# Optimization experiments

Hardware: AMD Instinct MI355X
Metric: run time of the kernel (lower is better)

The kernel has to match this reference:

```python
import jax, jax.numpy as jnp
import numpy as np

NEG = -1e9  # matches torch masked_fill value -1000000000.0


def setup_inputs() -> dict:
    key = jax.random.key(0)
    ks = jax.random.split(key, 8)
    B, n, m, d = 16, 1024, 128, 768
    C = jax.random.normal(ks[0], (B, n, d), jnp.float32)
    Q = jax.random.normal(ks[1], (B, m, d), jnp.float32)
    c_mask = jax.random.randint(ks[2], (B, 1, n), 0, 2).astype(bool)
    q_mask = jax.random.randint(ks[3], (B, 1, m), 0, 2).astype(bool)
    w1 = jax.random.normal(ks[4], (d,), jnp.float32)
    w2 = jax.random.normal(ks[5], (d,), jnp.float32)
    w3 = jax.random.normal(ks[6], (1, 1, d), jnp.float32)
    bias = jax.random.normal(ks[7], (1, 1), jnp.float32)
    return {"C": C, "Q": Q, "c_mask": c_mask, "q_mask": q_mask,
            "w1": w1, "w2": w2, "w3": w3, "bias": bias}


def reference(C, Q, c_mask, q_mask, w1, w2, w3, bias):
    # trilinear score S[b,i,j] = w1.C_i + w2.Q_j + (C_i * w3) . Q_j
    c_logit = jnp.einsum('bnd,d->bn', C, w1)[:, :, None]      # [B,n,1]
    q_logit = jnp.einsum('bmd,d->bm', Q, w2)[:, None, :]      # [B,1,m]
    dot_logit = jnp.einsum('bnd,bmd->bnm', C * w3, Q)         # [B,n,m]
    S = c_logit + q_logit + dot_logit                          # [B,n,m]

    # C2Q: mask padded query cols and padded context rows, softmax over query dim
    Sm = jnp.where(q_mask, NEG, S)                             # q_mask [B,1,m]
    Sm = jnp.where(jnp.swapaxes(c_mask, 1, 2), NEG, Sm)        # c_mask^T [B,n,1]
    C2Q = jax.nn.softmax(Sm, axis=-1)                          # [B,n,m]

    # Q2C: mask context cols of S^T, max over query dim, softmax over context dim
    St = jnp.where(c_mask, NEG, jnp.swapaxes(S, 1, 2))         # [B,m,n]
    q2c_logits = jnp.max(St, axis=1, keepdims=True)            # [B,1,n]
    Q2C = jax.nn.softmax(q2c_logits, axis=-1)                  # [B,1,n]

    A = jnp.einsum('bnm,bmd->bnd', C2Q, Q)                     # [B,n,d]
    # torch expands Q2C to [B,n,n] then bmm's with C; every row is identical,
    # so compute once and broadcast: [B,1,n] @ [B,n,d] -> [B,1,d]
    Bctx = jnp.einsum('bon,bnd->bod', Q2C, C)                  # [B,1,d]
    Bfull = jnp.broadcast_to(Bctx, C.shape)
    out = jnp.concatenate([C, A, C * A, C * Bfull], axis=-1)   # [B,n,4d]
    return out
```

## Files before the change

kernel.cpp:

```cpp
#include <hip/hip_runtime.h>
#include <math.h>
#include <stdint.h>

#define NEGV -1e9f
typedef float f32x4 __attribute__((ext_vector_type(4)));
typedef short bf16x8 __attribute__((ext_vector_type(8)));
typedef unsigned int u32x4 __attribute__((ext_vector_type(4)));

constexpr int B_ = 16, N_ = 1024, M_ = 128, D_ = 768;
constexpr int NCH = 12;

constexpr size_t OFF_QLOGP = 0;
constexpr size_t OFF_ROWMAX = 98304;
constexpr size_t OFF_BCTX   = 163840;
constexpr size_t OFF_WQ2C   = 212992;
constexpr size_t OFF_QIMG   = 278528;
constexpr size_t SZ_QIMG    = 3145728;
constexpr size_t WS_NEED    = OFF_QIMG + 4 * SZ_QIMG;

__device__ __forceinline__ unsigned short bf_rne(float x) {
    unsigned u = __float_as_uint(x);
    return (unsigned short)((u + 0x7fffu + ((u >> 16) & 1u)) >> 16);
}
__device__ __forceinline__ void splitf(float x, unsigned short& h, unsigned short& l) {
    unsigned short hb = bf_rne(x);
    float hf = __uint_as_float((unsigned)hb << 16);
    h = hb;
    l = bf_rne(x - hf);
}
__device__ __forceinline__ void gl_lds16(const void* g, void* l) {
    __builtin_amdgcn_global_load_lds(
        (const __attribute__((address_space(1))) void*)g,
        (__attribute__((address_space(3))) void*)l, 16, 0, 0);
}

__global__ __launch_bounds__(256) void k_prep(const float* __restrict__ Q,
                                              const float* __restrict__ w2,
                                              const float* __restrict__ w3,
                                              char* __restrict__ qwh, char* __restrict__ qwl,
                                              char* __restrict__ qth, char* __restrict__ qtl,
                                              float* __restrict__ qlogp) {
    int b = blockIdx.x / NCH, c = blockIdx.x % NCH;
    int t = threadIdx.x;
    __shared__ unsigned sT[128][66];
    __shared__ float sW2[64], sW3c[64];
    if (t < 64) sW2[t] = w2[c * 64 + t];
    else if (t < 128) sW3c[t - 64] = w3[c * 64 + (t - 64)];
    __syncthreads();
    int j = t >> 1, half = t & 1;
    const float* src = Q + ((size_t)(b * M_ + j)) * D_ + c * 64 + half * 32;
    unsigned short hs[32], ls[32];
    float qsum = 0.f;
#pragma unroll
    for (int u = 0; u < 8; ++u) {
        float4 v = *(const float4*)(src + u * 4);
        float f[4] = {v.x, v.y, v.z, v.w};
#pragma unroll
        for (int e = 0; e < 4; ++e) {
            int idx = u * 4 + e, d = half * 32 + idx;
            qsum += f[e] * sW2[d];
            unsigned short rh, rl; splitf(f[e], rh, rl);
            sT[j][d] = ((unsigned)rh << 16) | (unsigned)rl;
            unsigned short h, l; splitf(f[e] * sW3c[d], h, l);
            hs[idx] = h; ls[idx] = l;
        }
    }
    qsum += __shfl_xor(qsum, 1);
    if (half == 0) qlogp[(size_t)(b * M_ + j) * NCH + c] = qsum;
    size_t cb = ((size_t)(b * NCH + c)) * 16384;
    {
        int jh = j >> 6, jt = (j >> 4) & 3, c15j = j & 15;
#pragma unroll
        for (int u2 = 0; u2 < 4; ++u2) {
            int g = half * 4 + u2, ks = g >> 2, q4g = g & 3;
            int lane = q4g * 16 + c15j;
            bf16x8 hv, lv;
#pragma unroll
            for (int e = 0; e < 8; ++e) { hv[e] = (short)hs[u2 * 8 + e]; lv[e] = (short)ls[u2 * 8 + e]; }
            size_t off = cb + (size_t)((((jh * 2 + ks) * 4 + jt) * 64 + lane) * 16);
            *(bf16x8*)(qwh + off) = hv;
            *(bf16x8*)(qwl + off) = lv;
        }
    }
    __syncthreads();
#pragma unroll
    for (int u = 0; u < 4; ++u) {
        int id = t * 4 + u;
        int dd = id >> 4, gj = id & 15;
        int jh3 = dd >> 5, dt = (dd >> 4) & 1, c15q = dd & 15;
        int ks2 = gj >> 2, q4g = gj & 3;
        int lane = q4g * 16 + c15q;
        bf16x8 hv, lv;
#pragma unroll
        for (int e = 0; e < 8; ++e) {
            unsigned p = sT[gj * 8 + e][dd];
            hv[e] = (short)(p >> 16); lv[e] = (short)(p & 0xffffu);
        }
        size_t off = cb + (size_t)((((jh3 * 4 + ks2) * 2 + dt) * 64 + lane) * 16);
        *(bf16x8*)(qth + off) = hv;
        *(bf16x8*)(qtl + off) = lv;
    }
}

__global__ __launch_bounds__(256, 3) void k_main_v8(const float* __restrict__ C,
                                                    const int* __restrict__ c_mask,
                                                    const int* __restrict__ q_mask,
                                                    const float* __restrict__ w1,
                                                    const float* __restrict__ qlogp,
                                                    const char* __restrict__ qwh,
                                                    const char* __restrict__ qwl,
                                                    const char* __restrict__ qth,
                                                    const char* __restrict__ qtl,
                                                    float* __restrict__ rowmax,
                                                    float* __restrict__ out) {
    const int bid = (blockIdx.x & 7) * 64 + (blockIdx.x >> 3);
    const int b  = bid >> 5;
    const int r0 = (bid & 31) * 32;
    const int t  = threadIdx.x;
    const int wv = t >> 6, lane = t & 63;
    const int rg = wv >> 1, jh = wv & 1;
    const int q4 = lane >> 4, c15 = t & 15;

    const float* Cb = C + ((size_t)(b * N_ + r0)) * D_;

    __shared__ __align__(16) char uni[49152];
    __shared__ float sW1[D_];
    __shared__ float sQlog[M_];
    __shared__ int   sQmask[M_];
    __shared__ float sClog[32];
    __shared__ float sRedR[64], sRedM[64], sRedS[64];

    char* sQH  = uni;
    char* sQL  = uni + 16384;
    char* sQtH = uni;
    char* sQtL = uni + 16384;
    char* sPH  = uni + 32768;
    char* sPL  = uni + 40960;

    for (int k = t; k < D_; k += 256) sW1[k] = w1[k];
    if (t < M_) {
        const float* qp = qlogp + (size_t)(b * M_ + t) * NCH;
        float4 x = *(const float4*)qp, y = *(const float4*)(qp + 4), z = *(const float4*)(qp + 8);
        sQlog[t] = ((x.x + x.y) + (x.z + x.w)) + ((y.x + y.y) + (y.z + y.w)) +
                   ((z.x + z.y) + (z.z + z.w));
        sQmask[t] = q_mask[b * M_ + t];
    }
    __syncthreads();

    f32x4 acc[4] = {};
    float clogp = 0.f;
    const int arow = rg * 16 + c15;
    const float* CbA = Cb + (size_t)arow * D_;
    const size_t qcb = (size_t)(b * NCH) * 16384;

    for (int kidx = 0; kidx < NCH; ++kidx) {
        __syncthreads();
        {
            size_t gb = qcb + (size_t)kidx * 16384;
#pragma unroll
            for (int it = 0; it < 4; ++it) {
                int qo = it * 4096 + wv * 1024;
                gl_lds16(qwh + gb + qo + lane * 16, sQH + qo);
                gl_lds16(qwl + gb + qo + lane * 16, sQL + qo);
            }
        }
        bf16x8 ah[2], al[2];
        const int kb = kidx * 64;
#pragma unroll
        for (int ks = 0; ks < 2; ++ks) {
            const int k0 = kb + (ks * 4 + q4) * 8;
            float4 ca  = *(const float4*)(CbA + k0);
            float4 cb2 = *(const float4*)(CbA + k0 + 4);
            float cc[8] = {ca.x, ca.y, ca.z, ca.w, cb2.x, cb2.y, cb2.z, cb2.w};
#pragma unroll
            for (int e = 0; e < 8; ++e) {
                clogp += cc[e] * sW1[k0 + e];
                unsigned short h, l; splitf(cc[e], h, l);
                ah[ks][e] = (short)h; al[ks][e] = (short)l;
            }
        }
        __syncthreads();
#pragma unroll
        for (int ks = 0; ks < 2; ++ks) {
#pragma unroll
            for (int jt = 0; jt < 4; ++jt) {
                int fo = (((jh * 2 + ks) * 4 + jt) * 64 + lane) * 16;
                bf16x8 bh = *(const bf16x8*)(sQH + fo);
                bf16x8 bl = *(const bf16x8*)(sQL + fo);
                acc[jt] = __builtin_amdgcn_mfma_f32_16x16x32_bf16(ah[ks], bh, acc[jt], 0, 0, 0);
                acc[jt] = __builtin_amdgcn_mfma_f32_16x16x32_bf16(ah[ks], bl, acc[jt], 0, 0, 0);
                acc[jt] = __builtin_amdgcn_mfma_f32_16x16x32_bf16(al[ks], bh, acc[jt], 0, 0, 0);
            }
        }
    }
    clogp += __shfl_xor(clogp, 16);
    clogp += __shfl_xor(clogp, 32);
    if (jh == 0 && q4 == 0) sClog[arow] = clogp;
    __syncthreads();

    float qlg[4]; int qmv[4];
#pragma unroll
    for (int jt = 0; jt < 4; ++jt) {
        int j = jh * 64 + jt * 16 + c15;
        qlg[jt] = sQlog[j]; qmv[jt] = sQmask[j];
    }
    int cmv[4]; float clgr[4];
#pragma unroll
    for (int rr = 0; rr < 4; ++rr) {
        int row = rg * 16 + q4 * 4 + rr;
        cmv[rr]  = c_mask[b * N_ + r0 + row];
        clgr[rr] = sClog[row];
    }
    float mv[4][4], rmx[4], mmx[4];
#pragma unroll
    for (int rr = 0; rr < 4; ++rr) { rmx[rr] = -INFINITY; mmx[rr] = -INFINITY; }
#pragma unroll
    for (int jt = 0; jt < 4; ++jt)
#pragma unroll
        for (int rr = 0; rr < 4; ++rr) {
            float val = acc[jt][rr] + clgr[rr] + qlg[jt];
            float m   = (cmv[rr] | qmv[jt]) ? NEGV : val;
            mv[jt][rr] = m;
            rmx[rr] = fmaxf(rmx[rr], val);
            mmx[rr] = fmaxf(mmx[rr], m);
        }
#pragma unroll
    for (int rr = 0; rr < 4; ++rr)
#pragma unroll
        for (int off = 8; off; off >>= 1) {
            rmx[rr] = fmaxf(rmx[rr], __shfl_xor(rmx[rr], off));
            mmx[rr] = fmaxf(mmx[rr], __shfl_xor(mmx[rr], off));
        }
    if (c15 == 0) {
#pragma unroll
        for (int rr = 0; rr < 4; ++rr) {
            int row = rg * 16 + q4 * 4 + rr;
            sRedR[row * 2 + jh] = rmx[rr];
            sRedM[row * 2 + jh] = mmx[rr];
        }
    }
    __syncthreads();
    float Mm[4], sum[4];
#pragma unroll
    for (int rr = 0; rr < 4; ++rr) {
        int row = rg * 16 + q4 * 4 + rr;
        float Mraw = fmaxf(sRedR[row * 2], sRedR[row * 2 + 1]);
        Mm[rr] = fmaxf(sRedM[row * 2], sRedM[row * 2 + 1]);
        if (jh == 0 && c15 == 0) rowmax[b * N_ + r0 + row] = Mraw;
        sum[rr] = 0.f;
    }
    float p[4][4];
#pragma unroll
    for (int jt = 0; jt < 4; ++jt)
#pragma unroll
        for (int rr = 0; rr < 4; ++rr) {
            float e = __expf(mv[jt][rr] - Mm[rr]);
            p[jt][rr] = e; sum[rr] += e;
        }
#pragma unroll
    for (int rr = 0; rr < 4; ++rr) {
#pragma unroll
        for (int off = 8; off; off >>= 1) sum[rr] += __shfl_xor(sum[rr], off);
        if (c15 == 0) sRedS[(rg * 16 + q4 * 4 + rr) * 2 + jh] = sum[rr];
    }
    __syncthreads();
#pragma unroll
    for (int rr = 0; rr < 4; ++rr) {
        int row = rg * 16 + q4 * 4 + rr;
        float inv = 1.f / (sRedS[row * 2] + sRedS[row * 2 + 1]);
#pragma unroll
        for (int jt = 0; jt < 4; ++jt) {
            float P = p[jt][rr] * inv;
            unsigned short h, l; splitf(P, h, l);
            int j = jh * 64 + jt * 16 + c15;
            int addr = row * 256 + (((j >> 3) ^ (row & 7)) * 16) + (j & 7) * 2;
            *(short*)(sPH + addr) = (short)h;
            *(short*)(sPL + addr) = (short)l;
        }
    }
    __syncthreads();

    bf16x8 pah[4], pal[4];
    const int prow = rg * 16 + c15;
#pragma unroll
    for (int ks2 = 0; ks2 < 4; ++ks2) {
        int gja = ks2 * 4 + q4;
        int pgp = (gja ^ (prow & 7)) * 16;
        pah[ks2] = *(const bf16x8*)(sPH + prow * 256 + pgp);
        pal[ks2] = *(const bf16x8*)(sPL + prow * 256 + pgp);
    }
    for (int dc = 0; dc < NCH; ++dc) {
        __syncthreads();
        {
            size_t gb = qcb + (size_t)dc * 16384;
#pragma unroll
            for (int it = 0; it < 4; ++it) {
                int qo = it * 4096 + wv * 1024;
                gl_lds16(qth + gb + qo + lane * 16, sQtH + qo);
                gl_lds16(qtl + gb + qo + lane * 16, sQtL + qo);
            }
        }
        __syncthreads();
        f32x4 acc2[2] = {};
#pragma unroll
        for (int ks2 = 0; ks2 < 4; ++ks2) {
#pragma unroll
            for (int dt = 0; dt < 2; ++dt) {
                int fo = (((jh * 4 + ks2) * 2 + dt) * 64 + lane) * 16;
                bf16x8 bh = *(const bf16x8*)(sQtH + fo);
                bf16x8 bl = *(const bf16x8*)(sQtL + fo);
                acc2[dt] = __builtin_amdgcn_mfma_f32_16x16x32_bf16(pah[ks2], bh, acc2[dt], 0, 0, 0);
                acc2[dt] = __builtin_amdgcn_mfma_f32_16x16x32_bf16(pah[ks2], bl, acc2[dt], 0, 0, 0);
                acc2[dt] = __builtin_amdgcn_mfma_f32_16x16x32_bf16(pal[ks2], bh, acc2[dt], 0, 0, 0);
            }
        }
#pragma unroll
        for (int dt = 0; dt < 2; ++dt) {
            int dcol = dc * 64 + jh * 32 + dt * 16 + c15;
#pragma unroll
            for (int rr = 0; rr < 4; ++rr) {
                int row = rg * 16 + q4 * 4 + rr;
                float a = acc2[dt][rr];
                float c = Cb[(size_t)row * D_ + dcol];
                size_t ob = (size_t)(b * N_ + r0 + row) * 3072;
                out[ob + dcol] = c;
                out[ob + 768 + dcol] = a;
                out[ob + 1536 + dcol] = c * a;
            }
        }
    }
}

__global__ __launch_bounds__(256) void k_q2c(const float* __restrict__ rowmax,
                                             const int* __restrict__ c_mask,
                                             float* __restrict__ wq2c) {
    int b = blockIdx.x, t = threadIdx.x;
    __shared__ float red[8];
    float l[4];
#pragma unroll
    for (int u = 0; u < 4; ++u) {
        int i = t + u * 256;
        l[u] = (c_mask[b * N_ + i] != 0) ? NEGV : rowmax[b * N_ + i];
    }
    float mx = fmaxf(fmaxf(l[0], l[1]), fmaxf(l[2], l[3]));
#pragma unroll
    for (int off = 32; off; off >>= 1) mx = fmaxf(mx, __shfl_xor(mx, off));
    if ((t & 63) == 0) red[t >> 6] = mx;
    __syncthreads();
    mx = fmaxf(fmaxf(red[0], red[1]), fmaxf(red[2], red[3]));
    float e[4], s = 0.f;
#pragma unroll
    for (int u = 0; u < 4; ++u) { e[u] = __expf(l[u] - mx); s += e[u]; }
#pragma unroll
    for (int off = 32; off; off >>= 1) s += __shfl_xor(s, off);
    if ((t & 63) == 0) red[4 + (t >> 6)] = s;
    __syncthreads();
    s = red[4] + red[5] + red[6] + red[7];
    float inv = 1.f / s;
#pragma unroll
    for (int u = 0; u < 4; ++u) wq2c[b * N_ + t + u * 256] = e[u] * inv;
}

__global__ __launch_bounds__(256) void k_bctx(const float* __restrict__ C,
                                              const float* __restrict__ wq2c,
                                              float* __restrict__ Bctx) {
    int b  = blockIdx.x / 12;
    int c0 = (blockIdx.x % 12) * 64;
    int t  = threadIdx.x;
    int col = t & 63, ig = t >> 6;
    __shared__ float part[4][64];
    const float* wb = wq2c + b * N_;
    const float* Cb = C + (size_t)b * N_ * D_;
    float s = 0.f;
    for (int i = ig * 256; i < ig * 256 + 256; ++i)
        s += wb[i] * Cb[(size_t)i * D_ + c0 + col];
    part[ig][col] = s;
    __syncthreads();
    if (t < 64) Bctx[b * D_ + c0 + t] = part[0][t] + part[1][t] + part[2][t] + part[3][t];
}

__global__ __launch_bounds__(192) void k_final(const float* __restrict__ C,
                                               const float* __restrict__ Bctx,
                                               float* __restrict__ out) {
    int row = blockIdx.x;
    int b = row >> 10;
    int t = threadIdx.x;
    float4 c = *(const float4*)(C + (size_t)row * D_ + t * 4);
    float4 g = *(const float4*)(Bctx + (size_t)b * D_ + t * 4);
    *(float4*)(out + (size_t)row * 3072 + 2304 + t * 4) =
        make_float4(c.x * g.x, c.y * g.y, c.z * g.z, c.w * g.w);
}

__global__ __launch_bounds__(256) void k_qlogit(const float* __restrict__ Q,
                                                const float* __restrict__ w2,
                                                float* __restrict__ qlog) {
    int idx  = blockIdx.x * 4 + (threadIdx.x >> 6);
    int lane = threadIdx.x & 63;
    const float* q = Q + (size_t)idx * D_;
    float s = 0.f;
    for (int k = lane; k < D_; k += 64) s += q[k] * w2[k];
#pragma unroll
    for (int off = 32; off; off >>= 1) s += __shfl_xor(s, off);
    if (lane == 0) qlog[idx] = s;
}

__global__ __launch_bounds__(256, 2) void k_main_fb(const float* __restrict__ C,
                                                    const float* __restrict__ Q,
                                                    const int* __restrict__ c_mask,
                                                    const int* __restrict__ q_mask,
                                                    const float* __restrict__ w1,
                                                    const float* __restrict__ w3,
                                                    const float* __restrict__ qlog,
                                                    float* __restrict__ rowmax,
                                                    float* __restrict__ out) {
    const int bid = (blockIdx.x & 7) * 64 + (blockIdx.x >> 3);
    const int b  = bid >> 5;
    const int r0 = (bid & 31) * 32;
    const int t  = threadIdx.x;
    const int wv = t >> 6;
    const int rg = wv >> 1, jh = wv & 1;
    const int q4 = (t & 63) >> 4, c15 = t & 15;

    const float* Cb = C + ((size_t)(b * N_ + r0)) * D_;
    const float* Qb = Q + (size_t)b * M_ * D_;

    __shared__ __align__(16) char uni[49152];
    __shared__ float sW1[D_], sW3[D_];
    __shared__ float sQlog[M_];
    __shared__ int   sQmask[M_];
    __shared__ float sClog[32];
    __shared__ float sRedR[64], sRedM[64], sRedS[64];

    char* sCwH = uni;
    char* sCwL = uni + 4096;
    char* sQH  = uni + 8192;
    char* sQL  = uni + 24576;
    char* sPt  = uni;
    char* sQtP = uni + 16384;

    for (int k = t; k < D_; k += 256) { sW1[k] = w1[k]; sW3[k] = w3[k]; }
    if (t < M_) { sQlog[t] = qlog[b * M_ + t]; sQmask[t] = q_mask[b * M_ + t]; }

    f32x4 acc[4] = {};
    float clog = 0.f;
    const int cr = t >> 3, ckq = t & 7;
    const int qj = t >> 1, qk0 = (t & 1) * 32;

    for (int kb = 0; kb < D_; kb += 64) {
        __syncthreads();
        {
            const float* p = Cb + (size_t)cr * D_ + kb + ckq * 8;
            float4 a  = *(const float4*)p;
            float4 bb = *(const float4*)(p + 4);
            float cc[8] = {a.x, a.y, a.z, a.w, bb.x, bb.y, bb.z, bb.w};
            bf16x8 hv, lv;
            int kk = kb + ckq * 8;
#pragma unroll
            for (int e = 0; e < 8; ++e) {
                clog += cc[e] * sW1[kk + e];
                unsigned short h, l;
                splitf(cc[e] * sW3[kk + e], h, l);
                hv[e] = (short)h; lv[e] = (short)l;
            }
            int pg = (ckq ^ (cr & 7)) * 16;
            *(bf16x8*)(sCwH + cr * 128 + pg) = hv;
            *(bf16x8*)(sCwL + cr * 128 + pg) = lv;
        }
        {
            const float* p = Qb + (size_t)qj * D_ + kb + qk0;
#pragma unroll
            for (int u = 0; u < 4; ++u) {
                float4 a  = *(const float4*)(p + u * 8);
                float4 bb = *(const float4*)(p + u * 8 + 4);
                float qq[8] = {a.x, a.y, a.z, a.w, bb.x, bb.y, bb.z, bb.w};
                bf16x8 hv, lv;
#pragma unroll
                for (int e = 0; e < 8; ++e) {
                    unsigned short h, l;
                    splitf(qq[e], h, l);
                    hv[e] = (short)h; lv[e] = (short)l;
                }
                int g  = (t & 1) * 4 + u;
                int pg = (g ^ (qj & 7)) * 16;
                *(bf16x8*)(sQH + qj * 128 + pg) = hv;
                *(bf16x8*)(sQL + qj * 128 + pg) = lv;
            }
        }
        __syncthreads();
        const int arow = rg * 16 + c15;
#pragma unroll
        for (int ks = 0; ks < 2; ++ks) {
            int g  = ks * 4 + q4;
            int pg = (g ^ (c15 & 7)) * 16;
            bf16x8 ah = *(const bf16x8*)(sCwH + arow * 128 + pg);
            bf16x8 al = *(const bf16x8*)(sCwL + arow * 128 + pg);
#pragma unroll
            for (int jt = 0; jt < 4; ++jt) {
                int jr = jh * 64 + jt * 16 + c15;
                bf16x8 bh = *(const bf16x8*)(sQH + jr * 128 + pg);
                bf16x8 bl = *(const bf16x8*)(sQL + jr * 128 + pg);
                acc[jt] = __builtin_amdgcn_mfma_f32_16x16x32_bf16(ah, bh, acc[jt], 0, 0, 0);
                acc[jt] = __builtin_amdgcn_mfma_f32_16x16x32_bf16(ah, bl, acc[jt], 0, 0, 0);
                acc[jt] = __builtin_amdgcn_mfma_f32_16x16x32_bf16(al, bh, acc[jt], 0, 0, 0);
            }
        }
    }

    clog += __shfl_xor(clog, 1); clog += __shfl_xor(clog, 2); clog += __shfl_xor(clog, 4);
    if ((t & 7) == 0) sClog[cr] = clog;
    __syncthreads();

    float qlg[4]; int qmv[4];
#pragma unroll
    for (int jt = 0; jt < 4; ++jt) {
        int j = jh * 64 + jt * 16 + c15;
        qlg[jt] = sQlog[j]; qmv[jt] = sQmask[j];
    }
    int cmv[4]; float clgr[4];
#pragma unroll
    for (int rr = 0; rr < 4; ++rr) {
        int row = rg * 16 + q4 * 4 + rr;
        cmv[rr]  = c_mask[b * N_ + r0 + row];
        clgr[rr] = sClog[row];
    }
    float mv[4][4], rmx[4], mmx[4];
#pragma unroll
    for (int rr = 0; rr < 4; ++rr) { rmx[rr] = -INFINITY; mmx[rr] = -INFINITY; }
#pragma unroll
    for (int jt = 0; jt < 4; ++jt)
#pragma unroll
        for (int rr = 0; rr < 4; ++rr) {
            float val = acc[jt][rr] + clgr[rr] + qlg[jt];
            float m   = (cmv[rr] | qmv[jt]) ? NEGV : val;
            mv[jt][rr] = m;
            rmx[rr] = fmaxf(rmx[rr], val);
            mmx[rr] = fmaxf(mmx[rr], m);
        }
#pragma unroll
    for (int rr = 0; rr < 4; ++rr)
#pragma unroll
        for (int off = 8; off; off >>= 1) {
            rmx[rr] = fmaxf(rmx[rr], __shfl_xor(rmx[rr], off));
            mmx[rr] = fmaxf(mmx[rr], __shfl_xor(mmx[rr], off));
        }
    if (c15 == 0) {
#pragma unroll
        for (int rr = 0; rr < 4; ++rr) {
            int row = rg * 16 + q4 * 4 + rr;
            sRedR[row * 2 + jh] = rmx[rr];
            sRedM[row * 2 + jh] = mmx[rr];
        }
    }
    __syncthreads();
    float Mm[4], sum[4];
#pragma unroll
    for (int rr = 0; rr < 4; ++rr) {
        int row = rg * 16 + q4 * 4 + rr;
        float Mraw = fmaxf(sRedR[row * 2], sRedR[row * 2 + 1]);
        Mm[rr] = fmaxf(sRedM[row * 2], sRedM[row * 2 + 1]);
        if (jh == 0 && c15 == 0) rowmax[b * N_ + r0 + row] = Mraw;
        sum[rr] = 0.f;
    }
    float p[4][4];
#pragma unroll
    for (int jt = 0; jt < 4; ++jt)
#pragma unroll
        for (int rr = 0; rr < 4; ++rr) {
            float e = __expf(mv[jt][rr] - Mm[rr]);
            p[jt][rr] = e; sum[rr] += e;
        }
#pragma unroll
    for (int rr = 0; rr < 4; ++rr) {
#pragma unroll
        for (int off = 8; off; off >>= 1) sum[rr] += __shfl_xor(sum[rr], off);
        if (c15 == 0) sRedS[(rg * 16 + q4 * 4 + rr) * 2 + jh] = sum[rr];
    }
    __syncthreads();
#pragma unroll
    for (int rr = 0; rr < 4; ++rr) {
        int row = rg * 16 + q4 * 4 + rr;
        float inv = 1.f / (sRedS[row * 2] + sRedS[row * 2 + 1]);
#pragma unroll
        for (int jt = 0; jt < 4; ++jt) {
            float P = p[jt][rr] * inv;
            unsigned short h, l; splitf(P, h, l);
            unsigned pk = ((unsigned)h << 16) | (unsigned)l;
            int j  = jh * 64 + jt * 16 + c15;
            int gu = j >> 2;
            *(unsigned*)(sPt + row * 512 + ((gu ^ (row & 7)) * 16) + (j & 3) * 4) = pk;
        }
    }

    const int pj = t >> 1, pdh = (t & 1) * 32;
    for (int d0 = 0; d0 < D_; d0 += 64) {
        __syncthreads();
        {
            const float* p = Qb + (size_t)pj * D_ + d0 + pdh;
            int gu = pj >> 2, joff = (pj & 3) * 4;
#pragma unroll
            for (int u = 0; u < 8; ++u) {
                float4 a = *(const float4*)(p + u * 4);
                float qq[4] = {a.x, a.y, a.z, a.w};
#pragma unroll
                for (int e = 0; e < 4; ++e) {
                    unsigned short h, l; splitf(qq[e], h, l);
                    int d = pdh + u * 4 + e;
                    *(unsigned*)(sQtP + d * 512 + ((gu ^ (d & 7)) * 16) + joff) =
                        ((unsigned)h << 16) | (unsigned)l;
                }
            }
        }
        __syncthreads();
        f32x4 acc2[2] = {};
        const int prow = rg * 16 + c15;
#pragma unroll
        for (int ks2 = 0; ks2 < 4; ++ks2) {
            int gu0 = ks2 * 8 + q4 * 2;
            u32x4 pa = *(const u32x4*)(sPt + prow * 512 + ((gu0 ^ (c15 & 7)) * 16));
            u32x4 pb = *(const u32x4*)(sPt + prow * 512 + (((gu0 + 1) ^ (c15 & 7)) * 16));
            bf16x8 phi, plo;
#pragma unroll
            for (int e = 0; e < 4; ++e) {
                phi[e]     = (short)(pa[e] >> 16); plo[e]     = (short)(pa[e] & 0xffffu);
                phi[e + 4] = (short)(pb[e] >> 16); plo[e + 4] = (short)(pb[e] & 0xffffu);
            }
#pragma unroll
            for (int dt = 0; dt < 2; ++dt) {
                int dr = jh * 32 + dt * 16 + c15;
                u32x4 qa = *(const u32x4*)(sQtP + dr * 512 + ((gu0 ^ (dr & 7)) * 16));
                u32x4 qb = *(const u32x4*)(sQtP + dr * 512 + (((gu0 + 1) ^ (dr & 7)) * 16));
                bf16x8 bh, bl;
#pragma unroll
                for (int e = 0; e < 4; ++e) {
                    bh[e]     = (short)(qa[e] >> 16); bl[e]     = (short)(qa[e] & 0xffffu);
                    bh[e + 4] = (short)(qb[e] >> 16); bl[e + 4] = (short)(qb[e] & 0xffffu);
                }
                acc2[dt] = __builtin_amdgcn_mfma_f32_16x16x32_bf16(phi, bh, acc2[dt], 0, 0, 0);
                acc2[dt] = __builtin_amdgcn_mfma_f32_16x16x32_bf16(phi, bl, acc2[dt], 0, 0, 0);
                acc2[dt] = __builtin_amdgcn_mfma_f32_16x16x32_bf16(plo, bh, acc2[dt], 0, 0, 0);
            }
        }
#pragma unroll
        for (int dt = 0; dt < 2; ++dt)
#pragma unroll
            for (int rr = 0; rr < 4; ++rr) {
                int row  = rg * 16 + q4 * 4 + rr;
                int dcol = d0 + jh * 32 + dt * 16 + c15;
                float a = acc2[dt][rr];
                float c = Cb[(size_t)row * D_ + dcol];
                size_t ob = (size_t)(b * N_ + r0 + row) * 3072;
                out[ob + dcol] = c;
                out[ob + 768 + dcol] = a;
                out[ob + 1536 + dcol] = c * a;
            }
    }
}

extern "C" void kernel_launch(void* const* d_in, const int* in_sizes, int n_in,
                              void* d_out, int out_size, void* d_ws, size_t ws_size,
                              hipStream_t stream) {
    const float* C      = (const float*)d_in[0];
    const float* Q      = (const float*)d_in[1];
    const int*   c_mask = (const int*)d_in[2];
    const int*   q_mask = (const int*)d_in[3];
    const float* w1     = (const float*)d_in[4];
    const float* w2     = (const float*)d_in[5];
    const float* w3     = (const float*)d_in[6];
    float* out = (float*)d_out;
    char*  wsb = (char*)d_ws;

    float* qlogp  = (float*)(wsb + OFF_QLOGP);
    float* rowmax = (float*)(wsb + OFF_ROWMAX);
    float* bctx   = (float*)(wsb + OFF_BCTX);
    float* wq2c   = (float*)(wsb + OFF_WQ2C);

    if (ws_size >= WS_NEED) {
        char* qwh = wsb + OFF_QIMG;
        char* qwl = qwh + SZ_QIMG;
        char* qth = qwl + SZ_QIMG;
        char* qtl = qth + SZ_QIMG;
        k_prep<<<B_ * NCH, 256, 0, stream>>>(Q, w2, w3, qwh, qwl, qth, qtl, qlogp);
        k_main_v8<<<512, 256, 0, stream>>>(C, c_mask, q_mask, w1, qlogp,
                                           qwh, qwl, qth, qtl, rowmax, out);
    } else {
        float* qlog = (float*)(wsb + OFF_QLOGP);
        k_qlogit<<<512, 256, 0, stream>>>(Q, w2, qlog);
        k_main_fb<<<512, 256, 0, stream>>>(C, Q, c_mask, q_mask, w1, w3, qlog, rowmax, out);
    }
    k_q2c<<<16, 256, 0, stream>>>(rowmax, c_mask, wq2c);
    k_bctx<<<192, 256, 0, stream>>>(C, wq2c, bctx);
    k_final<<<16384, 192, 0, stream>>>(C, bctx, out);
}
```

Measured before the change: 112.5 us.

## Split main kernel and fuse Q2C softmax and C*Bctx output into pipeline

The main kernel is split in two. The first half computes scores and the C2Q probabilities, then writes the probability tile to workspace along with per-tile partial Q2C softmax sums (local max, denominator, weighted C rows). A small combine kernel merges the 32 partials per batch into Bctx with an online-softmax rescale. The second half reloads the probabilities, computes A, and writes all four output slices, including C*Bctx. This removes the separate k_q2c, k_bctx and k_final passes, which re-read C and rewrote a quarter of the output, at the cost of an extra kernel boundary and a round trip of the probability tile through global memory.

```diff
diff --git a/kernel.cpp b/kernel.cpp
--- a/kernel.cpp
+++ b/kernel.cpp
@@ -10,11 +10,13 @@
 constexpr int B_ = 16, N_ = 1024, M_ = 128, D_ = 768;
 constexpr int NCH = 12;
 
-constexpr size_t OFF_QLOGP = 0;
-constexpr size_t OFF_ROWMAX = 98304;
-constexpr size_t OFF_BCTX   = 163840;
+constexpr size_t OFF_QLOGP  = 0;
+constexpr size_t OFF_BCTX   = 98304;
+constexpr size_t OFF_PART   = 147456;
+constexpr size_t OFF_ROWMAX = 147456;
 constexpr size_t OFF_WQ2C   = 212992;
-constexpr size_t OFF_QIMG   = 278528;
+constexpr size_t OFF_PIMG   = 2244608;
+constexpr size_t OFF_QIMG   = 10633216;
 constexpr size_t SZ_QIMG    = 3145728;
 constexpr size_t WS_NEED    = OFF_QIMG + 4 * SZ_QIMG;
 
@@ -102,17 +104,15 @@
     }
 }
 
-__global__ __launch_bounds__(256, 3) void k_main_v8(const float* __restrict__ C,
-                                                    const int* __restrict__ c_mask,
-                                                    const int* __restrict__ q_mask,
-                                                    const float* __restrict__ w1,
-                                                    const float* __restrict__ qlogp,
-                                                    const char* __restrict__ qwh,
-                                                    const char* __restrict__ qwl,
-                                                    const char* __restrict__ qth,
-                                                    const char* __restrict__ qtl,
-                                                    float* __restrict__ rowmax,
-                                                    float* __restrict__ out) {
+__global__ __launch_bounds__(256, 3) void k_main1(const float* __restrict__ C,
+                                                  const int* __restrict__ c_mask,
+                                                  const int* __restrict__ q_mask,
+                                                  const float* __restrict__ w1,
+                                                  const float* __restrict__ qlogp,
+                                                  const char* __restrict__ qwh,
+                                                  const char* __restrict__ qwl,
+                                                  float* __restrict__ part,
+                                                  char* __restrict__ pimg) {
     const int bid = (blockIdx.x & 7) * 64 + (blockIdx.x >> 3);
     const int b  = bid >> 5;
     const int r0 = (bid & 31) * 32;
@@ -124,18 +124,16 @@
     const float* Cb = C + ((size_t)(b * N_ + r0)) * D_;
 
     __shared__ __align__(16) char uni[49152];
-    __shared__ float sW1[D_];
     __shared__ float sQlog[M_];
     __shared__ int   sQmask[M_];
-    __shared__ float sClog[32];
+    __shared__ float sClog[32], sMraw[32], sMl[32], sWr[32];
     __shared__ float sRedR[64], sRedM[64], sRedS[64];
 
-    char* sQH  = uni;
-    char* sQL  = uni + 16384;
-    char* sQtH = uni;
-    char* sQtL = uni + 16384;
-    char* sPH  = uni + 32768;
-    char* sPL  = uni + 40960;
+    char* sQH = uni;
+    char* sQL = uni + 16384;
+    char* sPH = uni + 32768;
+    char* sPL = uni + 40960;
+    float* sW1 = (float*)(uni + 32768);
 
     for (int k = t; k < D_; k += 256) sW1[k] = w1[k];
     if (t < M_) {
@@ -246,7 +244,7 @@
         int row = rg * 16 + q4 * 4 + rr;
         float Mraw = fmaxf(sRedR[row * 2], sRedR[row * 2 + 1]);
         Mm[rr] = fmaxf(sRedM[row * 2], sRedM[row * 2 + 1]);
-        if (jh == 0 && c15 == 0) rowmax[b * N_ + r0 + row] = Mraw;
+        if (jh == 0 && c15 == 0) sMraw[row] = Mraw;
         sum[rr] = 0.f;
     }
     float p[4][4];
@@ -280,6 +278,97 @@
     }
     __syncthreads();
 
+    if (t < 32) sMl[t] = (c_mask[b * N_ + r0 + t] != 0) ? NEGV : sMraw[t];
+    __syncthreads();
+    float lm = -INFINITY;
+#pragma unroll
+    for (int r = 0; r < 32; ++r) lm = fmaxf(lm, sMl[r]);
+    if (t < 32) sWr[t] = __expf(sMl[t] - lm);
+    __syncthreads();
+    float den = 0.f;
+#pragma unroll
+    for (int r = 0; r < 32; ++r) den += sWr[r];
+    {
+        float a0 = 0.f, a1 = 0.f, a2 = 0.f;
+        for (int r = 0; r < 32; ++r) {
+            float w = sWr[r];
+            const float* cr = Cb + (size_t)r * D_;
+            a0 += w * cr[t]; a1 += w * cr[t + 256]; a2 += w * cr[t + 512];
+        }
+        float* slot = part + (size_t)bid * 1024;
+        slot[2 + t] = a0; slot[2 + t + 256] = a1; slot[2 + t + 512] = a2;
+        if (t == 0) { slot[0] = lm; slot[1] = den; }
+    }
+#pragma unroll
+    for (int i = 0; i < 2; ++i) {
+        *(u32x4*)(pimg + (size_t)bid * 16384 + t * 32 + i * 16) =
+            *(const u32x4*)(sPH + t * 32 + i * 16);
+        *(u32x4*)(pimg + (size_t)bid * 16384 + 8192 + t * 32 + i * 16) =
+            *(const u32x4*)(sPL + t * 32 + i * 16);
+    }
+}
+
+__global__ __launch_bounds__(256) void k_combine(const float* __restrict__ part,
+                                                 float* __restrict__ bctx) {
+    int b = blockIdx.x, t = threadIdx.x;
+    __shared__ float sLm[32], sDen[32], sSc[32];
+    if (t < 32) {
+        const float* s = part + (size_t)(b * 32 + t) * 1024;
+        sLm[t] = s[0]; sDen[t] = s[1];
+    }
+    __syncthreads();
+    float gm = -INFINITY;
+#pragma unroll
+    for (int r = 0; r < 32; ++r) gm = fmaxf(gm, sLm[r]);
+    if (t < 32) sSc[t] = __expf(sLm[t] - gm);
+    __syncthreads();
+    float Ds = 0.f;
+#pragma unroll
+    for (int r = 0; r < 32; ++r) Ds += sDen[r] * sSc[r];
+    float inv = 1.f / Ds;
+#pragma unroll
+    for (int u = 0; u < 3; ++u) {
+        int col = t + u * 256;
+        float a = 0.f;
+        for (int rt = 0; rt < 32; ++rt)
+            a += sSc[rt] * part[(size_t)(b * 32 + rt) * 1024 + 2 + col];
+        bctx[b * D_ + col] = a * inv;
+    }
+}
+
+__global__ __launch_bounds__(256, 3) void k_main2(const float* __restrict__ C,
+                                                  const float* __restrict__ bctx,
+                                                  const char* __restrict__ qth,
+                                                  const char* __restrict__ qtl,
+                                                  const char* __restrict__ pimg,
+                                                  float* __restrict__ out) {
+    const int bid = (blockIdx.x & 7) * 64 + (blockIdx.x >> 3);
+    const int b  = bid >> 5;
+    const int r0 = (bid & 31) * 32;
+    const int t  = threadIdx.x;
+    const int wv = t >> 6, lane = t & 63;
+    const int rg = wv >> 1, jh = wv & 1;
+    const int q4 = lane >> 4, c15 = t & 15;
+
+    const float* Cb = C + ((size_t)(b * N_ + r0)) * D_;
+
+    __shared__ __align__(16) char uni[49152];
+    char* sQtH = uni;
+    char* sQtL = uni + 16384;
+    char* sPH  = uni + 32768;
+    char* sPL  = uni + 40960;
+
+    {
+        const char* ps = pimg + (size_t)bid * 16384;
+#pragma unroll
+        for (int it = 0; it < 2; ++it) {
+            int off = it * 4096 + wv * 1024;
+            gl_lds16(ps + off + lane * 16, sPH + off);
+            gl_lds16(ps + 8192 + off + lane * 16, sPL + off);
+        }
+    }
+    __syncthreads();
+
     bf16x8 pah[4], pal[4];
     const int prow = rg * 16 + c15;
 #pragma unroll
@@ -289,6 +378,8 @@
         pah[ks2] = *(const bf16x8*)(sPH + prow * 256 + pgp);
         pal[ks2] = *(const bf16x8*)(sPL + prow * 256 + pgp);
     }
+
+    const size_t qcb = (size_t)(b * NCH) * 16384;
     for (int dc = 0; dc < NCH; ++dc) {
         __syncthreads();
         {
@@ -317,6 +408,7 @@
 #pragma unroll
         for (int dt = 0; dt < 2; ++dt) {
             int dcol = dc * 64 + jh * 32 + dt * 16 + c15;
+            float g = bctx[b * D_ + dcol];
 #pragma unroll
             for (int rr = 0; rr < 4; ++rr) {
                 int row = rg * 16 + q4 * 4 + rr;
@@ -326,69 +418,10 @@
                 out[ob + dcol] = c;
                 out[ob + 768 + dcol] = a;
                 out[ob + 1536 + dcol] = c * a;
-            }
-        }
-    }
-}
-
-__global__ __launch_bounds__(256) void k_q2c(const float* __restrict__ rowmax,
-                                             const int* __restrict__ c_mask,
-                                             float* __restrict__ wq2c) {
-    int b = blockIdx.x, t = threadIdx.x;
-    __shared__ float red[8];
-    float l[4];
-#pragma unroll
-    for (int u = 0; u < 4; ++u) {
-        int i = t + u * 256;
-        l[u] = (c_mask[b * N_ + i] != 0) ? NEGV : rowmax[b * N_ + i];
-    }
-    float mx = fmaxf(fmaxf(l[0], l[1]), fmaxf(l[2], l[3]));
-#pragma unroll
-    for (int off = 32; off; off >>= 1) mx = fmaxf(mx, __shfl_xor(mx, off));
-    if ((t & 63) == 0) red[t >> 6] = mx;
-    __syncthreads();
-    mx = fmaxf(fmaxf(red[0], red[1]), fmaxf(red[2], red[3]));
-    float e[4], s = 0.f;
-#pragma unroll
-    for (int u = 0; u < 4; ++u) { e[u] = __expf(l[u] - mx); s += e[u]; }
-#pragma unroll
-    for (int off = 32; off; off >>= 1) s += __shfl_xor(s, off);
-    if ((t & 63) == 0) red[4 + (t >> 6)] = s;
-    __syncthreads();
-    s = red[4] + red[5] + red[6] + red[7];
-    float inv = 1.f / s;
-#pragma unroll
-    for (int u = 0; u < 4; ++u) wq2c[b * N_ + t + u * 256] = e[u] * inv;
-}
-
-__global__ __launch_bounds__(256) void k_bctx(const float* __restrict__ C,
-                                              const float* __restrict__ wq2c,
-                                              float* __restrict__ Bctx) {
-    int b  = blockIdx.x / 12;
-    int c0 = (blockIdx.x % 12) * 64;
-    int t  = threadIdx.x;
-    int col = t & 63, ig = t >> 6;
-    __shared__ float part[4][64];
-    const float* wb = wq2c + b * N_;
-    const float* Cb = C + (size_t)b * N_ * D_;
-    float s = 0.f;
-    for (int i = ig * 256; i < ig * 256 + 256; ++i)
-        s += wb[i] * Cb[(size_t)i * D_ + c0 + col];
-    part[ig][col] = s;
-    __syncthreads();
-    if (t < 64) Bctx[b * D_ + c0 + t] = part[0][t] + part[1][t] + part[2][t] + part[3][t];
-}
-
-__global__ __launch_bounds__(192) void k_final(const float* __restrict__ C,
-                                               const float* __restrict__ Bctx,
-                                               float* __restrict__ out) {
-    int row = blockIdx.x;
-    int b = row >> 10;
-    int t = threadIdx.x;
-    float4 c = *(const float4*)(C + (size_t)row * D_ + t * 4);
-    float4 g = *(const float4*)(Bctx + (size_t)b * D_ + t * 4);
-    *(float4*)(out + (size_t)row * 3072 + 2304 + t * 4) =
-        make_float4(c.x * g.x, c.y * g.y, c.z * g.z, c.w * g.w);
+                out[ob + 2304 + dcol] = c * g;
+            }
+        }
+    }
 }
 
 __global__ __launch_bounds__(256) void k_qlogit(const float* __restrict__ Q,
@@ -656,6 +689,66 @@
     }
 }
 
+__global__ __launch_bounds__(256) void k_q2c(const float* __restrict__ rowmax,
+                                             const int* __restrict__ c_mask,
+                                             float* __restrict__ wq2c) {
+    int b = blockIdx.x, t = threadIdx.x;
+    __shared__ float red[8];
+    float l[4];
+#pragma unroll
+    for (int u = 0; u < 4; ++u) {
+        int i = t + u * 256;
+        l[u] = (c_mask[b * N_ + i] != 0) ? NEGV : rowmax[b * N_ + i];
+    }
+    float mx = fmaxf(fmaxf(l[0], l[1]), fmaxf(l[2], l[3]));
+#pragma unroll
+    for (int off = 32; off; off >>= 1) mx = fmaxf(mx, __shfl_xor(mx, off));
+    if ((t & 63) == 0) red[t >> 6] = mx;
+    __syncthreads();
+    mx = fmaxf(fmaxf(red[0], red[1]), fmaxf(red[2], red[3]));
+    float e[4], s = 0.f;
+#pragma unroll
+    for (int u = 0; u < 4; ++u) { e[u] = __expf(l[u] - mx); s += e[u]; }
+#pragma unroll
+    for (int off = 32; off; off >>= 1) s += __shfl_xor(s, off);
+    if ((t & 63) == 0) red[4 + (t >> 6)] = s;
+    __syncthreads();
+    s = red[4] + red[5] + red[6] + red[7];
+    float inv = 1.f / s;
+#pragma unroll
+    for (int u = 0; u < 4; ++u) wq2c[b * N_ + t + u * 256] = e[u] * inv;
+}
+
+__global__ __launch_bounds__(256) void k_bctx(const float* __restrict__ C,
+                                              const float* __restrict__ wq2c,
+                                              float* __restrict__ Bctx) {
+    int b  = blockIdx.x / 12;
+    int c0 = (blockIdx.x % 12) * 64;
+    int t  = threadIdx.x;
+    int col = t & 63, ig = t >> 6;
+    __shared__ float part[4][64];
+    const float* wb = wq2c + b * N_;
+    const float* Cb = C + (size_t)b * N_ * D_;
+    float s = 0.f;
+    for (int i = ig * 256; i < ig * 256 + 256; ++i)
+        s += wb[i] * Cb[(size_t)i * D_ + c0 + col];
+    part[ig][col] = s;
+    __syncthreads();
+    if (t < 64) Bctx[b * D_ + c0 + t] = part[0][t] + part[1][t] + part[2][t] + part[3][t];
+}
+
+__global__ __launch_bounds__(192) void k_final(const float* __restrict__ C,
+                                               const float* __restrict__ Bctx,
+                                               float* __restrict__ out) {
+    int row = blockIdx.x;
+    int b = row >> 10;
+    int t = threadIdx.x;
+    float4 c = *(const float4*)(C + (size_t)row * D_ + t * 4);
+    float4 g = *(const float4*)(Bctx + (size_t)b * D_ + t * 4);
+    *(float4*)(out + (size_t)row * 3072 + 2304 + t * 4) =
+        make_float4(c.x * g.x, c.y * g.y, c.z * g.z, c.w * g.w);
+}
+
 extern "C" void kernel_launch(void* const* d_in, const int* in_sizes, int n_in,
                               void* d_out, int out_size, void* d_ws, size_t ws_size,
                               hipStream_t stream) {
@@ -670,9 +763,9 @@
     char*  wsb = (char*)d_ws;
 
     float* qlogp  = (float*)(wsb + OFF_QLOGP);
-    float* rowmax = (float*)(wsb + OFF_ROWMAX);
     float* bctx   = (float*)(wsb + OFF_BCTX);
-    float* wq2c   = (float*)(wsb + OFF_WQ2C);
+    float* part   = (float*)(wsb + OFF_PART);
+    char*  pimg   = wsb + OFF_PIMG;
 
     if (ws_size >= WS_NEED) {
         char* qwh = wsb + OFF_QIMG;
@@ -680,14 +773,17 @@
         char* qth = qwl + SZ_QIMG;
         char* qtl = qth + SZ_QIMG;
         k_prep<<<B_ * NCH, 256, 0, stream>>>(Q, w2, w3, qwh, qwl, qth, qtl, qlogp);
-        k_main_v8<<<512, 256, 0, stream>>>(C, c_mask, q_mask, w1, qlogp,
-                                           qwh, qwl, qth, qtl, rowmax, out);
+        k_main1<<<512, 256, 0, stream>>>(C, c_mask, q_mask, w1, qlogp, qwh, qwl, part, pimg);
+        k_combine<<<B_, 256, 0, stream>>>(part, bctx);
+        k_main2<<<512, 256, 0, stream>>>(C, bctx, qth, qtl, pimg, out);
     } else {
-        float* qlog = (float*)(wsb + OFF_QLOGP);
+        float* qlog   = (float*)(wsb + OFF_QLOGP);
+        float* rowmax = (float*)(wsb + OFF_ROWMAX);
+        float* wq2c   = (float*)(wsb + OFF_WQ2C);
         k_qlogit<<<512, 256, 0, stream>>>(Q, w2, qlog);
         k_main_fb<<<512, 256, 0, stream>>>(C, Q, c_mask, q_mask, w1, w3, qlog, rowmax, out);
-    }
-    k_q2c<<<16, 256, 0, stream>>>(rowmax, c_mask, wq2c);
-    k_bctx<<<192, 256, 0, stream>>>(C, wq2c, bctx);
-    k_final<<<16384, 192, 0, stream>>>(C, bctx, out);
-}
+        k_q2c<<<16, 256, 0, stream>>>(rowmax, c_mask, wq2c);
+        k_bctx<<<192, 256, 0, stream>>>(C, wq2c, bctx);
+        k_final<<<16384, 192, 0, stream>>>(C, bctx, out);
+    }
+}
```

After: 97.15 us. -13.6%, faster.
